# Kernel tuning notes

Hardware: AMD Instinct MI355X
Metric: run time of the kernel (lower is better)

## Reference

```python
import jax, jax.numpy as jnp
import numpy as np

VERY_NEG = -1e30


def setup_inputs() -> dict:
    key = jax.random.key(0)
    kq, kk, kv, km = jax.random.split(key, 4)
    B, H, S, D = 4, 8, 2048, 64
    Q = jax.random.normal(kq, (B, H, S, D), dtype=jnp.float32)
    K = jax.random.normal(kk, (B, H, S, D), dtype=jnp.float32)
    V = jax.random.normal(kv, (B, H, S, D), dtype=jnp.float32)
    # key-padding mask broadcast over heads and queries: 1 = keep, 0 = masked
    mask = jax.random.randint(km, (B, 1, 1, S), 0, 2, dtype=jnp.int32)
    return {"Q": Q, "K": K, "V": V, "mask": mask}


def reference(Q, K, V, mask):
    d_k = Q.shape[-1]
    scale = jnp.asarray(np.power(d_k, 0.5), dtype=Q.dtype)
    # scores: [B,H,S_q,S_k]
    scores = jnp.einsum("bhqd,bhkd->bhqk", Q, K) / scale
    # QANet exponential_mask: add -1e30 where mask == 0
    masked = scores + (1.0 - mask.astype(scores.dtype)) * VERY_NEG
    attn = jax.nn.softmax(masked, axis=-1)
    out = jnp.einsum("bhqk,bhkd->bhqd", attn, V)
    return out
```

## Files before the change

kernel.cpp:

```cpp
#include <hip/hip_runtime.h>

typedef _Float16 half8_t __attribute__((ext_vector_type(8)));
typedef _Float16 half4_t __attribute__((ext_vector_type(4)));
typedef _Float16 half2_t __attribute__((ext_vector_type(2)));
typedef __fp16 fp16x2 __attribute__((ext_vector_type(2)));
typedef float f32x4 __attribute__((ext_vector_type(4)));

#define S_LEN 2048
#define D_DIM 64
#define SD (S_LEN * D_DIM)
#define BC 64
#define NKT (S_LEN / BC)
#define LDK 72
#define LDO 68
#define THR 4.0f
#define WS_NEED ((size_t)16 * 1024 * 1024)

__global__ __launch_bounds__(256)
void prep_kernel(const float* __restrict__ Kg, const float* __restrict__ Vg,
                 _Float16* __restrict__ wsK, _Float16* __restrict__ wsV) {
  __shared__ float vt[64][68];
  const int blk = blockIdx.x;
  const int t = threadIdx.x;

  if (blk < 1024) {
    const int bh = blk >> 5, kt = blk & 31;
    const float* src = Kg + (size_t)bh * SD + (size_t)kt * BC * D_DIM;
    char* dst = (char*)wsK + (size_t)blk * 8192;
#pragma unroll
    for (int i = 0; i < 2; ++i) {
      int task = t + 256 * i;
      int row = task >> 3, j = task & 7;
      float4 lo = *(const float4*)(src + row * D_DIM + 8 * j);
      float4 hi = *(const float4*)(src + row * D_DIM + 8 * j + 4);
      fp16x2 p0 = __builtin_amdgcn_cvt_pkrtz(lo.x, lo.y);
      fp16x2 p1 = __builtin_amdgcn_cvt_pkrtz(lo.z, lo.w);
      fp16x2 p2 = __builtin_amdgcn_cvt_pkrtz(hi.x, hi.y);
      fp16x2 p3 = __builtin_amdgcn_cvt_pkrtz(hi.z, hi.w);
      half8_t h;
      h[0] = (_Float16)p0[0]; h[1] = (_Float16)p0[1];
      h[2] = (_Float16)p1[0]; h[3] = (_Float16)p1[1];
      h[4] = (_Float16)p2[0]; h[5] = (_Float16)p2[1];
      h[6] = (_Float16)p3[0]; h[7] = (_Float16)p3[1];
      *(half8_t*)(dst + row * 128 + ((16 * j) ^ ((row & 7) << 4))) = h;
    }
  } else {
    const int vb = blk - 1024;
    const int bh = vb >> 5, kt = vb & 31;
    const float* src = Vg + (size_t)bh * SD + (size_t)kt * BC * D_DIM;
#pragma unroll
    for (int i = 0; i < 4; ++i) {
      int r = (t >> 4) + 16 * i, c4 = t & 15;
      *(float4*)&vt[r][c4 * 4] = *(const float4*)(src + r * D_DIM + c4 * 4);
    }
    __syncthreads();
    char* dst = (char*)wsV + (size_t)vb * 8192;
#pragma unroll
    for (int i = 0; i < 4; ++i) {
      int task = t + 256 * i;
      int drow = task >> 4, j2 = task & 15, k0 = 4 * j2;
      float a = vt[k0][drow], b = vt[k0 + 1][drow];
      float cc = vt[k0 + 2][drow], d = vt[k0 + 3][drow];
      fp16x2 h0 = __builtin_amdgcn_cvt_pkrtz(a, b);
      fp16x2 h1 = __builtin_amdgcn_cvt_pkrtz(cc, d);
      half4_t h;
      h[0] = (_Float16)h0[0]; h[1] = (_Float16)h0[1];
      h[2] = (_Float16)h1[0]; h[3] = (_Float16)h1[1];
      *(half4_t*)(dst + drow * 128 + ((8 * j2) ^ ((drow & 15) << 3))) = h;
    }
  }
}

__global__ __launch_bounds__(256, 2)
void fattn_dma(const float* __restrict__ Qg, const _Float16* __restrict__ wsK,
               const _Float16* __restrict__ wsV, const int* __restrict__ Mg,
               float* __restrict__ Og) {
  __shared__ __align__(16) char smem[40960];
  float* Msh = (float*)(smem + 32768);
  float* Osh = (float*)smem;

  const int t = threadIdx.x;
  const int w = t >> 6;
  const int lane = t & 63;
  const int g = lane >> 4;
  const int c = lane & 15;

  const int bh = blockIdx.x & 31;
  const int qt = blockIdx.x >> 5;
  const int qb = qt * 128;

  const float* Qb = Qg + (size_t)bh * SD;
  const int*   Mb = Mg + (size_t)(bh >> 3) * S_LEN;
  float*       Ob = Og + (size_t)bh * SD;

  {
    int4 m0 = *(const int4*)(Mb + 8 * t);
    int4 m1 = *(const int4*)(Mb + 8 * t + 4);
    float4 f0, f1;
    f0.x = (float)(m0.x - 1) * 1e30f; f0.y = (float)(m0.y - 1) * 1e30f;
    f0.z = (float)(m0.z - 1) * 1e30f; f0.w = (float)(m0.w - 1) * 1e30f;
    f1.x = (float)(m1.x - 1) * 1e30f; f1.y = (float)(m1.y - 1) * 1e30f;
    f1.z = (float)(m1.z - 1) * 1e30f; f1.w = (float)(m1.w - 1) * 1e30f;
    *(float4*)(Msh + 8 * t) = f0;
    *(float4*)(Msh + 8 * t + 4) = f1;
  }

  const float qscale = 0.125f * 1.44269504088896340736f;
  half8_t qf[2][2];
#pragma unroll
  for (int h = 0; h < 2; ++h) {
    const float* qp = Qb + (size_t)(qb + 32 * w + 16 * h + c) * D_DIM + 8 * g;
#pragma unroll
    for (int ks = 0; ks < 2; ++ks) {
      float4 lo = *(const float4*)(qp + 32 * ks);
      float4 hi = *(const float4*)(qp + 32 * ks + 4);
      fp16x2 p0 = __builtin_amdgcn_cvt_pkrtz(lo.x * qscale, lo.y * qscale);
      fp16x2 p1 = __builtin_amdgcn_cvt_pkrtz(lo.z * qscale, lo.w * qscale);
      fp16x2 p2 = __builtin_amdgcn_cvt_pkrtz(hi.x * qscale, hi.y * qscale);
      fp16x2 p3 = __builtin_amdgcn_cvt_pkrtz(hi.z * qscale, hi.w * qscale);
      half8_t hh;
      hh[0] = (_Float16)p0[0]; hh[1] = (_Float16)p0[1];
      hh[2] = (_Float16)p1[0]; hh[3] = (_Float16)p1[1];
      hh[4] = (_Float16)p2[0]; hh[5] = (_Float16)p2[1];
      hh[6] = (_Float16)p3[0]; hh[7] = (_Float16)p3[1];
      qf[h][ks] = hh;
    }
  }

  const size_t tile_base0 = (size_t)bh * 32 * 8192;
  auto dma = [&](int buf, int kt) {
    const char* gK = (const char*)wsK + tile_base0 + (size_t)kt * 8192 +
                     w * 2048 + lane * 16;
    const char* gV = (const char*)wsV + tile_base0 + (size_t)kt * 8192 +
                     w * 2048 + lane * 16;
    char* lK = smem + 8192 * buf + w * 2048;
    char* lV = smem + 16384 + 8192 * buf + w * 2048;
    __builtin_amdgcn_global_load_lds((const float*)gK, (float*)lK, 16, 0, 0);
    __builtin_amdgcn_global_load_lds((const float*)(gK + 1024), (float*)(lK + 1024), 16, 0, 0);
    __builtin_amdgcn_global_load_lds((const float*)gV, (float*)lV, 16, 0, 0);
    __builtin_amdgcn_global_load_lds((const float*)(gV + 1024), (float*)(lV + 1024), 16, 0, 0);
  };

  f32x4 acc[2][4];
  f32x4 accl[2];
#pragma unroll
  for (int h = 0; h < 2; ++h) {
#pragma unroll
    for (int j = 0; j < 4; ++j) accl[h][j] = 0.f;
#pragma unroll
    for (int i = 0; i < 4; ++i)
#pragma unroll
      for (int j = 0; j < 4; ++j) acc[h][i][j] = 0.f;
  }
  float mrun[2] = {-1e30f, -1e30f};

  half4_t ones4;
  ones4[0] = (_Float16)1.0f; ones4[1] = (_Float16)1.0f;
  ones4[2] = (_Float16)1.0f; ones4[3] = (_Float16)1.0f;

  const int kxor = (c & 7) << 4;
  const int vxor = c << 3;

  dma(0, 0);
  __syncthreads();

  for (int kt = 0; kt < NKT; ++kt) {
    const int cur = kt & 1;
    if (kt < NKT - 1) dma(cur ^ 1, kt + 1);

    const char* Kc = smem + 8192 * cur;
    const char* Vc = smem + 16384 + 8192 * cur;

    f32x4 sT[2][4];
    __builtin_amdgcn_s_setprio(1);
#pragma unroll
    for (int mt = 0; mt < 4; ++mt) {
      f32x4 z0, z1;
#pragma unroll
      for (int j = 0; j < 4; ++j) { z0[j] = 0.f; z1[j] = 0.f; }
#pragma unroll
      for (int ks = 0; ks < 2; ++ks) {
        half8_t kf = *(const half8_t*)(Kc + (16 * mt + c) * 128 +
                                       ((ks * 64 + g * 16) ^ kxor));
        z0 = __builtin_amdgcn_mfma_f32_16x16x32_f16(kf, qf[0][ks], z0, 0, 0, 0);
        z1 = __builtin_amdgcn_mfma_f32_16x16x32_f16(kf, qf[1][ks], z1, 0, 0, 0);
      }
      sT[0][mt] = z0;
      sT[1][mt] = z1;
    }
    __builtin_amdgcn_s_setprio(0);

    half4_t vf[4][4];
#pragma unroll
    for (int dt = 0; dt < 4; ++dt)
#pragma unroll
      for (int mtk = 0; mtk < 4; ++mtk)
        vf[dt][mtk] = *(const half4_t*)(Vc + (16 * dt + c) * 128 +
                                        ((32 * mtk + 8 * g) ^ vxor));

    f32x4 mvf[4];
#pragma unroll
    for (int mt = 0; mt < 4; ++mt)
      mvf[mt] = *(const f32x4*)(Msh + kt * BC + 16 * mt + 4 * g);
#pragma unroll
    for (int h = 0; h < 2; ++h)
#pragma unroll
      for (int mt = 0; mt < 4; ++mt)
#pragma unroll
        for (int r = 0; r < 4; ++r) sT[h][mt][r] += mvf[mt][r];

    float tl[2];
#pragma unroll
    for (int h = 0; h < 2; ++h) {
      float tm0 = fmaxf(fmaxf(sT[h][0][0], sT[h][0][1]),
                        fmaxf(sT[h][0][2], sT[h][0][3]));
      float tm1 = fmaxf(fmaxf(sT[h][1][0], sT[h][1][1]),
                        fmaxf(sT[h][1][2], sT[h][1][3]));
      float tm2 = fmaxf(fmaxf(sT[h][2][0], sT[h][2][1]),
                        fmaxf(sT[h][2][2], sT[h][2][3]));
      float tm3 = fmaxf(fmaxf(sT[h][3][0], sT[h][3][1]),
                        fmaxf(sT[h][3][2], sT[h][3][3]));
      tl[h] = fmaxf(fmaxf(tm0, tm1), fmaxf(tm2, tm3));
    }
    int ok0 = __all(tl[0] <= mrun[0] + THR);
    int ok1 = __all(tl[1] <= mrun[1] + THR);
    if (!(ok0 & ok1)) {
#pragma unroll
      for (int h = 0; h < 2; ++h) {
        float tmax = tl[h];
        tmax = fmaxf(tmax, __shfl_xor(tmax, 16));
        tmax = fmaxf(tmax, __shfl_xor(tmax, 32));
        float mnew = fmaxf(mrun[h], tmax);
        float alpha = __builtin_amdgcn_exp2f(mrun[h] - mnew);
        mrun[h] = mnew;
        accl[h][0] *= alpha; accl[h][1] *= alpha;
        accl[h][2] *= alpha; accl[h][3] *= alpha;
#pragma unroll
        for (int mt = 0; mt < 4; ++mt) {
          acc[h][mt][0] *= alpha; acc[h][mt][1] *= alpha;
          acc[h][mt][2] *= alpha; acc[h][mt][3] *= alpha;
        }
      }
    }

    __builtin_amdgcn_s_setprio(1);
#pragma unroll
    for (int h = 0; h < 2; ++h) {
#pragma unroll
      for (int mt = 0; mt < 4; ++mt) {
        float pv0 = __builtin_amdgcn_exp2f(sT[h][mt][0] - mrun[h]);
        float pv1 = __builtin_amdgcn_exp2f(sT[h][mt][1] - mrun[h]);
        float pv2 = __builtin_amdgcn_exp2f(sT[h][mt][2] - mrun[h]);
        float pv3 = __builtin_amdgcn_exp2f(sT[h][mt][3] - mrun[h]);
        fp16x2 p01 = __builtin_amdgcn_cvt_pkrtz(pv0, pv1);
        fp16x2 p23 = __builtin_amdgcn_cvt_pkrtz(pv2, pv3);
        half4_t pf;
        pf[0] = (_Float16)p01[0]; pf[1] = (_Float16)p01[1];
        pf[2] = (_Float16)p23[0]; pf[3] = (_Float16)p23[1];
        accl[h] = __builtin_amdgcn_mfma_f32_16x16x16f16(ones4, pf, accl[h], 0, 0, 0);
#pragma unroll
        for (int dt = 0; dt < 4; ++dt)
          acc[h][dt] = __builtin_amdgcn_mfma_f32_16x16x16f16(vf[dt][mt], pf,
                                                             acc[h][dt], 0, 0, 0);
      }
    }
    __builtin_amdgcn_s_setprio(0);

    __syncthreads();
  }

#pragma unroll
  for (int h = 0; h < 2; ++h) {
    float linv = 1.f / accl[h][0];
#pragma unroll
    for (int mt = 0; mt < 4; ++mt)
#pragma unroll
      for (int r = 0; r < 4; ++r)
        Osh[(32 * w + 16 * h + c) * LDO + 16 * mt + 4 * g + r] = acc[h][mt][r] * linv;
  }
  __syncthreads();
  {
    int f8 = t & 7;
#pragma unroll
    for (int i = 0; i < 4; ++i) {
      int q = (t >> 3) + 32 * i;
#pragma unroll
      for (int j = 0; j < 2; ++j) {
        int c4 = f8 + 8 * j;
        f32x4 o = *(f32x4*)(Osh + q * LDO + c4 * 4);
        *(float4*)(Ob + (size_t)(qb + q) * D_DIM + c4 * 4) =
            make_float4(o.x, o.y, o.z, o.w);
      }
    }
  }
}

__global__ __launch_bounds__(256, 2)
void fattn_fb(const float* __restrict__ Qg, const float* __restrict__ Kg,
              const float* __restrict__ Vg, const int* __restrict__ Mg,
              float* __restrict__ Og) {
  __shared__ __align__(16) char smem[45056];
  float* Msh = (float*)(smem + 36864);
  float* Osh = (float*)smem;

  const int t = threadIdx.x;
  const int w = t >> 6;
  const int lane = t & 63;
  const int g = lane >> 4;
  const int c = lane & 15;

  const int bh = blockIdx.x & 31;
  const int qt = blockIdx.x >> 5;
  const int qb = qt * 128;

  const float* Qb = Qg + (size_t)bh * SD;
  const float* Kb = Kg + (size_t)bh * SD;
  const float* Vb = Vg + (size_t)bh * SD;
  const int*   Mb = Mg + (size_t)(bh >> 3) * S_LEN;
  float*       Ob = Og + (size_t)bh * SD;

  {
    int4 m0 = *(const int4*)(Mb + 8 * t);
    int4 m1 = *(const int4*)(Mb + 8 * t + 4);
    float4 f0, f1;
    f0.x = (float)(m0.x - 1) * 1e30f; f0.y = (float)(m0.y - 1) * 1e30f;
    f0.z = (float)(m0.z - 1) * 1e30f; f0.w = (float)(m0.w - 1) * 1e30f;
    f1.x = (float)(m1.x - 1) * 1e30f; f1.y = (float)(m1.y - 1) * 1e30f;
    f1.z = (float)(m1.z - 1) * 1e30f; f1.w = (float)(m1.w - 1) * 1e30f;
    *(float4*)(Msh + 8 * t) = f0;
    *(float4*)(Msh + 8 * t + 4) = f1;
  }

  const float qscale = 0.125f * 1.44269504088896340736f;
  half8_t qf[2][2];
#pragma unroll
  for (int h = 0; h < 2; ++h) {
    const float* qp = Qb + (size_t)(qb + 32 * w + 16 * h + c) * D_DIM + 8 * g;
#pragma unroll
    for (int ks = 0; ks < 2; ++ks) {
      float4 lo = *(const float4*)(qp + 32 * ks);
      float4 hi = *(const float4*)(qp + 32 * ks + 4);
      fp16x2 p0 = __builtin_amdgcn_cvt_pkrtz(lo.x * qscale, lo.y * qscale);
      fp16x2 p1 = __builtin_amdgcn_cvt_pkrtz(lo.z * qscale, lo.w * qscale);
      fp16x2 p2 = __builtin_amdgcn_cvt_pkrtz(hi.x * qscale, hi.y * qscale);
      fp16x2 p3 = __builtin_amdgcn_cvt_pkrtz(hi.z * qscale, hi.w * qscale);
      half8_t hh;
      hh[0] = (_Float16)p0[0]; hh[1] = (_Float16)p0[1];
      hh[2] = (_Float16)p1[0]; hh[3] = (_Float16)p1[1];
      hh[4] = (_Float16)p2[0]; hh[5] = (_Float16)p2[1];
      hh[6] = (_Float16)p3[0]; hh[7] = (_Float16)p3[1];
      qf[h][ks] = hh;
    }
  }

  const int krow0 = t >> 4;
  const int kc4   = t & 15;
  const int vp    = t >> 3;
  const int vkpl  = t & 7;

  float4 kr[4];
  float2 vr[8];
  auto prefetch = [&](int kb2) {
#pragma unroll
    for (int it = 0; it < 4; ++it)
      kr[it] = *(const float4*)(Kb + (size_t)(kb2 + krow0 + 16 * it) * D_DIM + kc4 * 4);
#pragma unroll
    for (int kc = 0; kc < 4; ++kc) {
      const float* vpp = Vb + (size_t)(kb2 + 2 * (vkpl + 8 * kc)) * D_DIM + 2 * vp;
      vr[2 * kc]     = *(const float2*)(vpp);
      vr[2 * kc + 1] = *(const float2*)(vpp + D_DIM);
    }
  };
  auto stage = [&](int buf) {
    _Float16* Kd = (_Float16*)(smem + 9216 * buf);
    _Float16* Vd = (_Float16*)(smem + 18432 + 9216 * buf);
#pragma unroll
    for (int it = 0; it < 4; ++it) {
      fp16x2 a  = __builtin_amdgcn_cvt_pkrtz(kr[it].x, kr[it].y);
      fp16x2 b2 = __builtin_amdgcn_cvt_pkrtz(kr[it].z, kr[it].w);
      half4_t h;
      h[0] = (_Float16)a[0]; h[1] = (_Float16)a[1];
      h[2] = (_Float16)b2[0]; h[3] = (_Float16)b2[1];
      *(half4_t*)(Kd + (krow0 + 16 * it) * LDK + kc4 * 4) = h;
    }
#pragma unroll
    for (int kc = 0; kc < 4; ++kc) {
      int kp = vkpl + 8 * kc;
      fp16x2 h0 = __builtin_amdgcn_cvt_pkrtz(vr[2 * kc].x, vr[2 * kc + 1].x);
      fp16x2 h1 = __builtin_amdgcn_cvt_pkrtz(vr[2 * kc].y, vr[2 * kc + 1].y);
      half2_t g0; g0[0] = (_Float16)h0[0]; g0[1] = (_Float16)h0[1];
      half2_t g1; g1[0] = (_Float16)h1[0]; g1[1] = (_Float16)h1[1];
      *(half2_t*)(Vd + (2 * vp) * LDK + 2 * kp) = g0;
      *(half2_t*)(Vd + (2 * vp + 1) * LDK + 2 * kp) = g1;
    }
  };

  f32x4 acc[2][4];
  f32x4 accl[2];
#pragma unroll
  for (int h = 0; h < 2; ++h) {
#pragma unroll
    for (int j = 0; j < 4; ++j) accl[h][j] = 0.f;
#pragma unroll
    for (int i = 0; i < 4; ++i)
#pragma unroll
      for (int j = 0; j < 4; ++j) acc[h][i][j] = 0.f;
  }
  float mrun[2] = {-1e30f, -1e30f};

  half4_t ones4;
  ones4[0] = (_Float16)1.0f; ones4[1] = (_Float16)1.0f;
  ones4[2] = (_Float16)1.0f; ones4[3] = (_Float16)1.0f;

  prefetch(0);
  stage(0);
  prefetch(BC);
  __syncthreads();

  for (int kt = 0; kt < NKT; ++kt) {
    const int kb = kt * BC;
    const int cur = kt & 1;

    if (kt < NKT - 1) stage(cur ^ 1);
    if (kt < NKT - 2) prefetch(kb + 2 * BC);

    const _Float16* Kc = (const _Float16*)(smem + 9216 * cur);
    const _Float16* Vc = (const _Float16*)(smem + 18432 + 9216 * cur);

    f32x4 sT[2][4];
    __builtin_amdgcn_s_setprio(1);
#pragma unroll
    for (int mt = 0; mt < 4; ++mt) {
      f32x4 z0, z1;
#pragma unroll
      for (int j = 0; j < 4; ++j) { z0[j] = 0.f; z1[j] = 0.f; }
#pragma unroll
      for (int ks = 0; ks < 2; ++ks) {
        half8_t kf = *(half8_t*)(Kc + (16 * mt + c) * LDK + ks * 32 + 8 * g);
        z0 = __builtin_amdgcn_mfma_f32_16x16x32_f16(kf, qf[0][ks], z0, 0, 0, 0);
        z1 = __builtin_amdgcn_mfma_f32_16x16x32_f16(kf, qf[1][ks], z1, 0, 0, 0);
      }
      sT[0][mt] = z0;
      sT[1][mt] = z1;
    }
    __builtin_amdgcn_s_setprio(0);

    half4_t vf[4][4];
#pragma unroll
    for (int dt = 0; dt < 4; ++dt)
#pragma unroll
      for (int kst = 0; kst < 4; ++kst)
        vf[dt][kst] = *(half4_t*)(Vc + (16 * dt + c) * LDK + 16 * kst + 4 * g);

    f32x4 mvf[4];
#pragma unroll
    for (int mt = 0; mt < 4; ++mt)
      mvf[mt] = *(const f32x4*)(Msh + kb + 16 * mt + 4 * g);
#pragma unroll
    for (int h = 0; h < 2; ++h)
#pragma unroll
      for (int mt = 0; mt < 4; ++mt)
#pragma unroll
        for (int r = 0; r < 4; ++r) sT[h][mt][r] += mvf[mt][r];

    float tl[2];
#pragma unroll
    for (int h = 0; h < 2; ++h) {
      float tm0 = fmaxf(fmaxf(sT[h][0][0], sT[h][0][1]),
                        fmaxf(sT[h][0][2], sT[h][0][3]));
      float tm1 = fmaxf(fmaxf(sT[h][1][0], sT[h][1][1]),
                        fmaxf(sT[h][1][2], sT[h][1][3]));
      float tm2 = fmaxf(fmaxf(sT[h][2][0], sT[h][2][1]),
                        fmaxf(sT[h][2][2], sT[h][2][3]));
      float tm3 = fmaxf(fmaxf(sT[h][3][0], sT[h][3][1]),
                        fmaxf(sT[h][3][2], sT[h][3][3]));
      tl[h] = fmaxf(fmaxf(tm0, tm1), fmaxf(tm2, tm3));
    }
    int ok0 = __all(tl[0] <= mrun[0] + THR);
    int ok1 = __all(tl[1] <= mrun[1] + THR);
    if (!(ok0 & ok1)) {
#pragma unroll
      for (int h = 0; h < 2; ++h) {
        float tmax = tl[h];
        tmax = fmaxf(tmax, __shfl_xor(tmax, 16));
        tmax = fmaxf(tmax, __shfl_xor(tmax, 32));
        float mnew = fmaxf(mrun[h], tmax);
        float alpha = __builtin_amdgcn_exp2f(mrun[h] - mnew);
        mrun[h] = mnew;
        accl[h][0] *= alpha; accl[h][1] *= alpha;
        accl[h][2] *= alpha; accl[h][3] *= alpha;
#pragma unroll
        for (int mt = 0; mt < 4; ++mt) {
          acc[h][mt][0] *= alpha; acc[h][mt][1] *= alpha;
          acc[h][mt][2] *= alpha; acc[h][mt][3] *= alpha;
        }
      }
    }

    __builtin_amdgcn_s_setprio(1);
#pragma unroll
    for (int h = 0; h < 2; ++h) {
#pragma unroll
      for (int mt = 0; mt < 4; ++mt) {
        float pv0 = __builtin_amdgcn_exp2f(sT[h][mt][0] - mrun[h]);
        float pv1 = __builtin_amdgcn_exp2f(sT[h][mt][1] - mrun[h]);
        float pv2 = __builtin_amdgcn_exp2f(sT[h][mt][2] - mrun[h]);
        float pv3 = __builtin_amdgcn_exp2f(sT[h][mt][3] - mrun[h]);
        fp16x2 p01 = __builtin_amdgcn_cvt_pkrtz(pv0, pv1);
        fp16x2 p23 = __builtin_amdgcn_cvt_pkrtz(pv2, pv3);
        half4_t pf;
        pf[0] = (_Float16)p01[0]; pf[1] = (_Float16)p01[1];
        pf[2] = (_Float16)p23[0]; pf[3] = (_Float16)p23[1];
        accl[h] = __builtin_amdgcn_mfma_f32_16x16x16f16(ones4, pf, accl[h], 0, 0, 0);
#pragma unroll
        for (int dt = 0; dt < 4; ++dt)
          acc[h][dt] = __builtin_amdgcn_mfma_f32_16x16x16f16(vf[dt][mt], pf,
                                                             acc[h][dt], 0, 0, 0);
      }
    }
    __builtin_amdgcn_s_setprio(0);

    __syncthreads();
  }

#pragma unroll
  for (int h = 0; h < 2; ++h) {
    float linv = 1.f / accl[h][0];
#pragma unroll
    for (int mt = 0; mt < 4; ++mt)
#pragma unroll
      for (int r = 0; r < 4; ++r)
        Osh[(32 * w + 16 * h + c) * LDO + 16 * mt + 4 * g + r] = acc[h][mt][r] * linv;
  }
  __syncthreads();
  {
    int f8 = t & 7;
#pragma unroll
    for (int i = 0; i < 4; ++i) {
      int q = (t >> 3) + 32 * i;
#pragma unroll
      for (int j = 0; j < 2; ++j) {
        int c4 = f8 + 8 * j;
        f32x4 o = *(f32x4*)(Osh + q * LDO + c4 * 4);
        *(float4*)(Ob + (size_t)(qb + q) * D_DIM + c4 * 4) =
            make_float4(o.x, o.y, o.z, o.w);
      }
    }
  }
}

extern "C" void kernel_launch(void* const* d_in, const int* in_sizes, int n_in,
                              void* d_out, int out_size, void* d_ws, size_t ws_size,
                              hipStream_t stream) {
  (void)in_sizes; (void)n_in; (void)out_size;
  const float* Q = (const float*)d_in[0];
  const float* K = (const float*)d_in[1];
  const float* V = (const float*)d_in[2];
  const int*   M = (const int*)d_in[3];
  float* O = (float*)d_out;

  if (ws_size >= WS_NEED && d_ws != nullptr) {
    _Float16* wsK = (_Float16*)d_ws;
    _Float16* wsV = wsK + (size_t)32 * S_LEN * D_DIM;
    prep_kernel<<<dim3(2048), dim3(256), 0, stream>>>(K, V, wsK, wsV);
    fattn_dma<<<dim3(32 * 16), dim3(256), 0, stream>>>(Q, wsK, wsV, M, O);
  } else {
    fattn_fb<<<dim3(32 * 16), dim3(256), 0, stream>>>(Q, K, V, M, O);
  }
}
```

Before: 142.2 us.

## Compact unmasked keys so attention loops only over valid key tiles

Adds a prefix-sum kernel that packs the indices of kept keys for each batch. The prep kernel gathers only those K/V rows into fp16 tiles and zero-fills the tail. The attention kernel then iterates over ceil(L/64) tiles instead of all 32, and drops the additive mask. Masked keys contribute exactly zero in the reference, so the work saved scales with the masked fraction; the costs are an extra launch, gathered non-contiguous reads, and a tail-tile row-sum fix-up.

```diff
diff --git a/kernel.cpp b/kernel.cpp
--- a/kernel.cpp
+++ b/kernel.cpp
@@ -10,48 +10,110 @@
 #define D_DIM 64
 #define SD (S_LEN * D_DIM)
 #define BC 64
-#define NKT (S_LEN / BC)
 #define LDK 72
 #define LDO 68
 #define THR 4.0f
-#define WS_NEED ((size_t)16 * 1024 * 1024)
+#define WS_NEED ((size_t)(16 * 1024 * 1024) + (size_t)4 * S_LEN * 4 + 64)
+
+
+__global__ __launch_bounds__(256)
+void compact_kernel(const int* __restrict__ Mg, int* __restrict__ idxp,
+                    int* __restrict__ Lp) {
+  __shared__ int pre[256];
+  const int b = blockIdx.x;
+  const int t = threadIdx.x;
+  const int* m = Mg + (size_t)b * S_LEN + 8 * t;
+  int4 m0 = *(const int4*)m;
+  int4 m1 = *(const int4*)(m + 4);
+  int v0 = m0.x, v1 = m0.y, v2 = m0.z, v3 = m0.w;
+  int v4 = m1.x, v5 = m1.y, v6 = m1.z, v7 = m1.w;
+  int c = v0 + v1 + v2 + v3 + v4 + v5 + v6 + v7;
+  pre[t] = c;
+  __syncthreads();
+  for (int off = 1; off < 256; off <<= 1) {
+    int x = (t >= off) ? pre[t - off] : 0;
+    __syncthreads();
+    pre[t] += x;
+    __syncthreads();
+  }
+  int pos = pre[t] - c;
+  int* dst = idxp + (size_t)b * S_LEN;
+  int base = 8 * t;
+  if (v0) dst[pos++] = base + 0;
+  if (v1) dst[pos++] = base + 1;
+  if (v2) dst[pos++] = base + 2;
+  if (v3) dst[pos++] = base + 3;
+  if (v4) dst[pos++] = base + 4;
+  if (v5) dst[pos++] = base + 5;
+  if (v6) dst[pos++] = base + 6;
+  if (v7) dst[pos++] = base + 7;
+  if (t == 255) Lp[b] = pre[255];
+}
 
 __global__ __launch_bounds__(256)
 void prep_kernel(const float* __restrict__ Kg, const float* __restrict__ Vg,
+                 const int* __restrict__ idxp, const int* __restrict__ Lp,
                  _Float16* __restrict__ wsK, _Float16* __restrict__ wsV) {
   __shared__ float vt[64][68];
+  __shared__ int ridx[64];
   const int blk = blockIdx.x;
   const int t = threadIdx.x;
 
   if (blk < 1024) {
-    const int bh = blk >> 5, kt = blk & 31;
-    const float* src = Kg + (size_t)bh * SD + (size_t)kt * BC * D_DIM;
+    const int bh = blk >> 5, kt = blk & 31, b = bh >> 3;
+    const int L = Lp[b];
+    int NT = (L + 63) >> 6; if (NT < 1) NT = 1;
+    if (kt >= NT) return;
+    if (t < 64) {
+      int j = kt * 64 + t;
+      ridx[t] = (j < L) ? idxp[(size_t)b * S_LEN + j] : -1;
+    }
+    __syncthreads();
+    const float* srcB = Kg + (size_t)bh * SD;
     char* dst = (char*)wsK + (size_t)blk * 8192;
 #pragma unroll
     for (int i = 0; i < 2; ++i) {
       int task = t + 256 * i;
       int row = task >> 3, j = task & 7;
-      float4 lo = *(const float4*)(src + row * D_DIM + 8 * j);
-      float4 hi = *(const float4*)(src + row * D_DIM + 8 * j + 4);
-      fp16x2 p0 = __builtin_amdgcn_cvt_pkrtz(lo.x, lo.y);
-      fp16x2 p1 = __builtin_amdgcn_cvt_pkrtz(lo.z, lo.w);
-      fp16x2 p2 = __builtin_amdgcn_cvt_pkrtz(hi.x, hi.y);
-      fp16x2 p3 = __builtin_amdgcn_cvt_pkrtz(hi.z, hi.w);
+      int sr = ridx[row];
       half8_t h;
-      h[0] = (_Float16)p0[0]; h[1] = (_Float16)p0[1];
-      h[2] = (_Float16)p1[0]; h[3] = (_Float16)p1[1];
-      h[4] = (_Float16)p2[0]; h[5] = (_Float16)p2[1];
-      h[6] = (_Float16)p3[0]; h[7] = (_Float16)p3[1];
+      if (sr >= 0) {
+        const float* src = srcB + (size_t)sr * D_DIM + 8 * j;
+        float4 lo = *(const float4*)(src);
+        float4 hi = *(const float4*)(src + 4);
+        fp16x2 p0 = __builtin_amdgcn_cvt_pkrtz(lo.x, lo.y);
+        fp16x2 p1 = __builtin_amdgcn_cvt_pkrtz(lo.z, lo.w);
+        fp16x2 p2 = __builtin_amdgcn_cvt_pkrtz(hi.x, hi.y);
+        fp16x2 p3 = __builtin_amdgcn_cvt_pkrtz(hi.z, hi.w);
+        h[0] = (_Float16)p0[0]; h[1] = (_Float16)p0[1];
+        h[2] = (_Float16)p1[0]; h[3] = (_Float16)p1[1];
+        h[4] = (_Float16)p2[0]; h[5] = (_Float16)p2[1];
+        h[6] = (_Float16)p3[0]; h[7] = (_Float16)p3[1];
+      } else {
+#pragma unroll
+        for (int e = 0; e < 8; ++e) h[e] = (_Float16)0.0f;
+      }
       *(half8_t*)(dst + row * 128 + ((16 * j) ^ ((row & 7) << 4))) = h;
     }
   } else {
     const int vb = blk - 1024;
-    const int bh = vb >> 5, kt = vb & 31;
-    const float* src = Vg + (size_t)bh * SD + (size_t)kt * BC * D_DIM;
+    const int bh = vb >> 5, kt = vb & 31, b = bh >> 3;
+    const int L = Lp[b];
+    int NT = (L + 63) >> 6; if (NT < 1) NT = 1;
+    if (kt >= NT) return;
+    if (t < 64) {
+      int j = kt * 64 + t;
+      ridx[t] = (j < L) ? idxp[(size_t)b * S_LEN + j] : -1;
+    }
+    __syncthreads();
+    const float* srcB = Vg + (size_t)bh * SD;
 #pragma unroll
     for (int i = 0; i < 4; ++i) {
       int r = (t >> 4) + 16 * i, c4 = t & 15;
-      *(float4*)&vt[r][c4 * 4] = *(const float4*)(src + r * D_DIM + c4 * 4);
+      int sr = ridx[r];
+      float4 val = make_float4(0.f, 0.f, 0.f, 0.f);
+      if (sr >= 0) val = *(const float4*)(srcB + (size_t)sr * D_DIM + c4 * 4);
+      *(float4*)&vt[r][c4 * 4] = val;
     }
     __syncthreads();
     char* dst = (char*)wsV + (size_t)vb * 8192;
@@ -59,9 +121,9 @@
     for (int i = 0; i < 4; ++i) {
       int task = t + 256 * i;
       int drow = task >> 4, j2 = task & 15, k0 = 4 * j2;
-      float a = vt[k0][drow], b = vt[k0 + 1][drow];
+      float a = vt[k0][drow], b2 = vt[k0 + 1][drow];
       float cc = vt[k0 + 2][drow], d = vt[k0 + 3][drow];
-      fp16x2 h0 = __builtin_amdgcn_cvt_pkrtz(a, b);
+      fp16x2 h0 = __builtin_amdgcn_cvt_pkrtz(a, b2);
       fp16x2 h1 = __builtin_amdgcn_cvt_pkrtz(cc, d);
       half4_t h;
       h[0] = (_Float16)h0[0]; h[1] = (_Float16)h0[1];
@@ -73,10 +135,9 @@
 
 __global__ __launch_bounds__(256, 2)
 void fattn_dma(const float* __restrict__ Qg, const _Float16* __restrict__ wsK,
-               const _Float16* __restrict__ wsV, const int* __restrict__ Mg,
+               const _Float16* __restrict__ wsV, const int* __restrict__ Lp,
                float* __restrict__ Og) {
-  __shared__ __align__(16) char smem[40960];
-  float* Msh = (float*)(smem + 32768);
+  __shared__ __align__(16) char smem[36864];
   float* Osh = (float*)smem;
 
   const int t = threadIdx.x;
@@ -90,20 +151,19 @@
   const int qb = qt * 128;
 
   const float* Qb = Qg + (size_t)bh * SD;
-  const int*   Mb = Mg + (size_t)(bh >> 3) * S_LEN;
   float*       Ob = Og + (size_t)bh * SD;
 
-  {
-    int4 m0 = *(const int4*)(Mb + 8 * t);
-    int4 m1 = *(const int4*)(Mb + 8 * t + 4);
-    float4 f0, f1;
-    f0.x = (float)(m0.x - 1) * 1e30f; f0.y = (float)(m0.y - 1) * 1e30f;
-    f0.z = (float)(m0.z - 1) * 1e30f; f0.w = (float)(m0.w - 1) * 1e30f;
-    f1.x = (float)(m1.x - 1) * 1e30f; f1.y = (float)(m1.y - 1) * 1e30f;
-    f1.z = (float)(m1.z - 1) * 1e30f; f1.w = (float)(m1.w - 1) * 1e30f;
-    *(float4*)(Msh + 8 * t) = f0;
-    *(float4*)(Msh + 8 * t + 4) = f1;
-  }
+  const int L = Lp[bh >> 3];
+  int NT = (L + 63) >> 6; if (NT < 1) NT = 1;
+
+  half4_t kAtail[4];
+#pragma unroll
+  for (int mt = 0; mt < 4; ++mt)
+#pragma unroll
+    for (int e = 0; e < 4; ++e) {
+      int j = (NT - 1) * 64 + 16 * mt + 4 * g + e;
+      kAtail[mt][e] = (_Float16)((j < L) ? 1.0f : 0.0f);
+    }
 
   const float qscale = 0.125f * 1.44269504088896340736f;
   half8_t qf[2][2];
@@ -164,9 +224,9 @@
   dma(0, 0);
   __syncthreads();
 
-  for (int kt = 0; kt < NKT; ++kt) {
+  for (int kt = 0; kt < NT; ++kt) {
     const int cur = kt & 1;
-    if (kt < NKT - 1) dma(cur ^ 1, kt + 1);
+    if (kt < NT - 1) dma(cur ^ 1, kt + 1);
 
     const char* Kc = smem + 8192 * cur;
     const char* Vc = smem + 16384 + 8192 * cur;
@@ -197,17 +257,6 @@
       for (int mtk = 0; mtk < 4; ++mtk)
         vf[dt][mtk] = *(const half4_t*)(Vc + (16 * dt + c) * 128 +
                                         ((32 * mtk + 8 * g) ^ vxor));
-
-    f32x4 mvf[4];
-#pragma unroll
-    for (int mt = 0; mt < 4; ++mt)
-      mvf[mt] = *(const f32x4*)(Msh + kt * BC + 16 * mt + 4 * g);
-#pragma unroll
-    for (int h = 0; h < 2; ++h)
-#pragma unroll
-      for (int mt = 0; mt < 4; ++mt)
-#pragma unroll
-        for (int r = 0; r < 4; ++r) sT[h][mt][r] += mvf[mt][r];
 
     float tl[2];
 #pragma unroll
@@ -243,6 +292,7 @@
       }
     }
 
+    const int isTail = (kt == NT - 1);
     __builtin_amdgcn_s_setprio(1);
 #pragma unroll
     for (int h = 0; h < 2; ++h) {
@@ -257,7 +307,8 @@
         half4_t pf;
         pf[0] = (_Float16)p01[0]; pf[1] = (_Float16)p01[1];
         pf[2] = (_Float16)p23[0]; pf[3] = (_Float16)p23[1];
-        accl[h] = __builtin_amdgcn_mfma_f32_16x16x16f16(ones4, pf, accl[h], 0, 0, 0);
+        half4_t ka = isTail ? kAtail[mt] : ones4;
+        accl[h] = __builtin_amdgcn_mfma_f32_16x16x16f16(ka, pf, accl[h], 0, 0, 0);
 #pragma unroll
         for (int dt = 0; dt < 4; ++dt)
           acc[h][dt] = __builtin_amdgcn_mfma_f32_16x16x16f16(vf[dt][mt], pf,
@@ -271,7 +322,8 @@
 
 #pragma unroll
   for (int h = 0; h < 2; ++h) {
-    float linv = 1.f / accl[h][0];
+    float denom = accl[h][0];
+    float linv = (denom != 0.f) ? 1.f / denom : 0.f;
 #pragma unroll
     for (int mt = 0; mt < 4; ++mt)
 #pragma unroll
@@ -417,12 +469,12 @@
   prefetch(BC);
   __syncthreads();
 
-  for (int kt = 0; kt < NKT; ++kt) {
+  for (int kt = 0; kt < 32; ++kt) {
     const int kb = kt * BC;
     const int cur = kt & 1;
 
-    if (kt < NKT - 1) stage(cur ^ 1);
-    if (kt < NKT - 2) prefetch(kb + 2 * BC);
+    if (kt < 31) stage(cur ^ 1);
+    if (kt < 30) prefetch(kb + 2 * BC);
 
     const _Float16* Kc = (const _Float16*)(smem + 9216 * cur);
     const _Float16* Vc = (const _Float16*)(smem + 18432 + 9216 * cur);
@@ -561,9 +613,12 @@
 
   if (ws_size >= WS_NEED && d_ws != nullptr) {
     _Float16* wsK = (_Float16*)d_ws;
-    _Float16* wsV = wsK + (size_t)32 * S_LEN * D_DIM;
-    prep_kernel<<<dim3(2048), dim3(256), 0, stream>>>(K, V, wsK, wsV);
-    fattn_dma<<<dim3(32 * 16), dim3(256), 0, stream>>>(Q, wsK, wsV, M, O);
+    _Float16* wsV = (_Float16*)((char*)d_ws + (size_t)8 * 1024 * 1024);
+    int* idxp = (int*)((char*)d_ws + (size_t)16 * 1024 * 1024);
+    int* Lp = idxp + 4 * S_LEN;
+    compact_kernel<<<dim3(4), dim3(256), 0, stream>>>(M, idxp, Lp);
+    prep_kernel<<<dim3(2048), dim3(256), 0, stream>>>(K, V, idxp, Lp, wsK, wsV);
+    fattn_dma<<<dim3(32 * 16), dim3(256), 0, stream>>>(Q, wsK, wsV, Lp, O);
   } else {
     fattn_fb<<<dim3(32 * 16), dim3(256), 0, stream>>>(Q, K, V, M, O);
   }
```

New measurement: 122.2 us. 1.16x faster.
